# Performance work log

Hardware: AMD Instinct MI355X
Metric: run time of the kernel (lower is better)

## Reference

```python
import jax, jax.numpy as jnp
import numpy as np

B, I, T = 256, 64, 16
V, E, H = 4096, 256, 256


def setup_inputs() -> dict:
    key = jax.random.key(0)
    ks = jax.random.split(key, 12)
    emb = jax.random.normal(ks[0], (V, E), jnp.float32) * 0.02
    emb = emb.at[0].set(0.0)  # padding_idx=0
    s_e = 1.0 / np.sqrt(H)
    inp = {
        "batched_blocks": jax.random.randint(ks[1], (B, I, T), 0, V, jnp.int32),
        "actual_instr_counts": jax.random.randint(ks[2], (B,), 1, I + 1, jnp.int32),
        "actual_token_counts": jax.random.randint(ks[3], (B, I), 0, T + 1, jnp.int32),
        "embedding": emb,
        "Wih_tok": jax.random.uniform(ks[4], (4 * H, E), jnp.float32, -s_e, s_e),
        "Whh_tok": jax.random.uniform(ks[5], (4 * H, H), jnp.float32, -s_e, s_e),
        "b_tok": jax.random.uniform(ks[6], (4 * H,), jnp.float32, -s_e, s_e),
        "Wih_ins": jax.random.uniform(ks[7], (4 * H, H), jnp.float32, -s_e, s_e),
        "Whh_ins": jax.random.uniform(ks[8], (4 * H, H), jnp.float32, -s_e, s_e),
        "b_ins": jax.random.uniform(ks[9], (4 * H,), jnp.float32, -s_e, s_e),
        "linW": jax.random.uniform(ks[10], (1, H), jnp.float32, -s_e, s_e),
        "linb": jax.random.uniform(ks[11], (1,), jnp.float32, -s_e, s_e),
    }
    return inp


def _lstm_last(x, lengths, Wih, Whh, b):
    # x: [N, T, D]; returns hidden state at step lengths-1 (zeros if length==0),
    # matching pack_padded_sequence -> LSTM -> h_n semantics.
    N, Tt, _ = x.shape
    Hh = Whh.shape[1]

    def step(carry, xt):
        h, c = carry
        g = xt @ Wih.T + h @ Whh.T + b  # [N, 4H], torch gate order i,f,g,o
        i, f, gg, o = jnp.split(g, 4, axis=-1)
        c = jax.nn.sigmoid(f) * c + jax.nn.sigmoid(i) * jnp.tanh(gg)
        h = jax.nn.sigmoid(o) * jnp.tanh(c)
        return (h, c), h

    h0 = jnp.zeros((N, Hh), x.dtype)
    _, hs = jax.lax.scan(step, (h0, h0), jnp.swapaxes(x, 0, 1))  # [T, N, H]
    hs = jnp.swapaxes(hs, 0, 1)  # [N, T, H]
    idx = jnp.clip(lengths - 1, 0, Tt - 1).astype(jnp.int32)
    h_last = jnp.take_along_axis(hs, jnp.broadcast_to(idx[:, None, None], (N, 1, Hh)), axis=1)[:, 0]
    return jnp.where((lengths > 0)[:, None], h_last, jnp.zeros_like(h_last))


def reference(batched_blocks, actual_instr_counts, actual_token_counts,
              embedding, Wih_tok, Whh_tok, b_tok, Wih_ins, Whh_ins, b_ins,
              linW, linb):
    Bb, Ii, Tt = batched_blocks.shape
    tok_flat = batched_blocks.reshape(Bb * Ii, Tt)
    emb = embedding[tok_flat]  # [B*I, T, E]
    tok_len = actual_token_counts.reshape(-1)
    instr_repr = _lstm_last(emb, tok_len, Wih_tok, Whh_tok, b_tok)  # [B*I, H]
    instr_repr = instr_repr.reshape(Bb, Ii, -1)
    block_repr = _lstm_last(instr_repr, actual_instr_counts, Wih_ins, Whh_ins, b_ins)  # [B, H]
    return block_repr @ linW.T + linb  # [B, 1]
```

## Files before the change

kernel.cpp:

```cpp
#include <hip/hip_runtime.h>
#include <hip/hip_bf16.h>

#define Bq 256
#define Iq 64
#define Tq 16
#define Vq 4096
#define Eq 256
#define Hq 256
#define NSEQ 16384
#define HSTR 264
#define HR 272
#define HBUF 4352
#define CL 8
#define XCC_GETREG_IMM 6164

typedef __attribute__((ext_vector_type(8))) __bf16 bf16x8;
typedef __attribute__((ext_vector_type(8))) short short8;
typedef __attribute__((ext_vector_type(4))) float f32x4;

__device__ __forceinline__ bf16x8 as_bf8(short8 v) {
    union { short8 s; bf16x8 b; } u; u.s = v; return u.b;
}
__device__ __forceinline__ float sigf(float x) {
    return __builtin_amdgcn_rcpf(1.f + __expf(-x));
}
__device__ __forceinline__ float tanh_fast(float x) {
    float e = __expf(2.f * x);
    return 1.f - 2.f * __builtin_amdgcn_rcpf(e + 1.f);
}
__device__ __forceinline__ short bf16_rne(float x) {
    unsigned u = __float_as_uint(x);
    unsigned r = (u + 0x7fffu + ((u >> 16) & 1u)) >> 16;
    return (short)r;
}
__device__ __forceinline__ float bf16f(short h) {
    return __uint_as_float(((unsigned)(unsigned short)h) << 16);
}
__device__ __forceinline__ void gl_lds16(const unsigned* g, unsigned* l) {
    __builtin_amdgcn_global_load_lds(
        (const __attribute__((address_space(1))) void*)g,
        (__attribute__((address_space(3))) void*)l, 16, 0, 1);
}

__global__ void k_pack(const float* __restrict__ Wih_tok,
                       const float* __restrict__ b_tok,
                       const float* __restrict__ b_ins,
                       float* __restrict__ Wih4t,
                       float* __restrict__ b4t, float* __restrict__ b4i) {
    int g = blockIdx.x;
    int q = g >> 8;
    int j = g & 255;
    int k = threadIdx.x;
    Wih4t[(k * 256 + j) * 4 + q] = Wih_tok[g * Hq + k];
    if (k == 0) {
        b4t[j * 4 + q] = b_tok[g];
        b4i[j * 4 + q] = b_ins[g];
    }
}

__global__ void k_packB(const float* __restrict__ W0,
                        const float* __restrict__ W1,
                        short* __restrict__ B0h, short* __restrict__ B0l,
                        short* __restrict__ B1h, short* __restrict__ B1l) {
    int nt = blockIdx.x;
    int kc = blockIdx.y;
    int l  = threadIdx.x;
    int n = nt * 16 + (l & 15);
    int kb = kc * 32 + (l >> 4) * 8;
    size_t ob = ((size_t)(nt * 8 + kc) * 64 + l) * 8;
    #pragma unroll
    for (int m = 0; m < 8; ++m) {
        float v = W0[n * 256 + kb + m];
        short hi = bf16_rne(v);
        B0h[ob + m] = hi; B0l[ob + m] = bf16_rne(v - bf16f(hi));
        v = W1[n * 256 + kb + m];
        hi = bf16_rne(v);
        B1h[ob + m] = hi; B1l[ob + m] = bf16_rne(v - bf16f(hi));
    }
}

__global__ void k_packB2(const float* __restrict__ W2,
                         short* __restrict__ B2h, short* __restrict__ B2l) {
    int bx = blockIdx.x;
    int kc = blockIdx.y;
    int l  = threadIdx.x;
    int j  = bx >> 3, nt = bx & 7;
    int n_local = nt * 16 + (l & 15);
    int gate = n_local & 3;
    int u = j * 32 + (n_local >> 2);
    int row = gate * 256 + u;
    int kb = kc * 32 + (l >> 4) * 8;
    size_t ob = ((size_t)(bx * 8 + kc) * 64 + l) * 8;
    #pragma unroll
    for (int m = 0; m < 8; ++m) {
        float v = W2[row * 256 + kb + m];
        short hi = bf16_rne(v);
        B2h[ob + m] = hi;
        B2l[ob + m] = bf16_rne(v - bf16f(hi));
    }
}

__global__ __launch_bounds__(1024) void k_sortn(const int* __restrict__ len,
                                                int* __restrict__ perm,
                                                int n, int nbins) {
    __shared__ int cnt[65];
    __shared__ int base[65];
    int tid = threadIdx.x;
    if (tid < nbins) cnt[tid] = 0;
    __syncthreads();
    for (int i = tid; i < n; i += 1024) atomicAdd(&cnt[len[i]], 1);
    __syncthreads();
    if (tid == 0) {
        int acc = 0;
        for (int b = nbins - 1; b >= 0; --b) { base[b] = acc; acc += cnt[b]; }
    }
    __syncthreads();
    for (int i = tid; i < n; i += 1024) {
        int pos = atomicAdd(&base[len[i]], 1);
        perm[pos] = i;
    }
}

__global__ void k_zero(int* __restrict__ p, int n) {
    int i = blockIdx.x * blockDim.x + threadIdx.x;
    if (i < n) p[i] = 0;
}

__global__ __launch_bounds__(256) void k_epre(const float* __restrict__ emb,
                                              const float4* __restrict__ Wih4t,
                                              const float4* __restrict__ b4t,
                                              float4* __restrict__ Ep4) {
    __shared__ float es[8][Eq];
    int tid = threadIdx.x;
    int v0 = blockIdx.x * 8;
    #pragma unroll
    for (int r = 0; r < 8; ++r) es[r][tid] = emb[(v0 + r) * Eq + tid];
    __syncthreads();
    float4 a[8];
    #pragma unroll
    for (int r = 0; r < 8; ++r) a[r] = make_float4(0.f, 0.f, 0.f, 0.f);
    const float4* Wp = Wih4t + tid;
    #pragma unroll 2
    for (int k = 0; k < Eq; ++k) {
        float4 wv = Wp[k * 256];
        #pragma unroll
        for (int r = 0; r < 8; ++r) {
            float e = es[r][k];
            a[r].x += wv.x * e; a[r].y += wv.y * e;
            a[r].z += wv.z * e; a[r].w += wv.w * e;
        }
    }
    float4 b4 = b4t[tid];
    #pragma unroll
    for (int r = 0; r < 8; ++r) {
        Ep4[(size_t)(v0 + r) * 256 + tid] =
            make_float4(a[r].x + b4.x, a[r].y + b4.y, a[r].z + b4.z, a[r].w + b4.w);
    }
}

#define MFMA3(accv, ah, al, bh, bl) \
    accv = __builtin_amdgcn_mfma_f32_16x16x32_bf16(ah, bh, accv, 0, 0, 0); \
    accv = __builtin_amdgcn_mfma_f32_16x16x32_bf16(al, bh, accv, 0, 0, 0); \
    accv = __builtin_amdgcn_mfma_f32_16x16x32_bf16(ah, bl, accv, 0, 0, 0);

__global__ __launch_bounds__(512) void k_token_mfma(
        const int* __restrict__ tokens,
        const int* __restrict__ tok_len,
        const int* __restrict__ perm,
        const float4* __restrict__ Ep4,
        const short* __restrict__ Bhi, const short* __restrict__ Blo,
        const short* __restrict__ BXhi, const short* __restrict__ BXlo,
        const float4* __restrict__ b4i,
        float4* __restrict__ Xp4) {
    __shared__ __align__(16) short hb[2][32 * HSTR];
    __shared__ int toks[32][Tq];
    __shared__ int lens[32];
    __shared__ int sid[32];
    int tid  = threadIdx.x;
    int w    = tid >> 6;
    int lane = tid & 63;
    int l15  = lane & 15;
    int quad = lane >> 4;
    int s0   = blockIdx.x * 32;

    if (tid < 32) {
        int q = perm[s0 + tid];
        sid[tid]  = q;
        lens[tid] = tok_len[q];
    }
    {
        int* hz = (int*)&hb[0][0];
        for (int i = tid; i < 32 * HSTR; i += 512) hz[i] = 0;
    }
    __syncthreads();
    toks[tid >> 4][tid & 15] = tokens[sid[tid >> 4] * Tq + (tid & 15)];
    int lenr[2][4], sidr[2][4];
    #pragma unroll
    for (int mt = 0; mt < 2; ++mt)
        #pragma unroll
        for (int r = 0; r < 4; ++r) {
            lenr[mt][r] = lens[mt * 16 + quad * 4 + r];
            sidr[mt][r] = sid[mt * 16 + quad * 4 + r];
        }
    int tmax = 0;
    #pragma unroll
    for (int s = 0; s < 32; ++s) tmax = max(tmax, lens[s]);
    __syncthreads();

    f32x4 acc[2][4][2];
    float cst[2][2][4], hst[2][2][4];
    #pragma unroll
    for (int u2 = 0; u2 < 2; ++u2)
        #pragma unroll
        for (int mt = 0; mt < 2; ++mt)
            #pragma unroll
            for (int r = 0; r < 4; ++r) { cst[u2][mt][r] = 0.f; hst[u2][mt][r] = 0.f; }

    for (int t = 0; t < tmax; ++t) {
        #pragma unroll
        for (int u2 = 0; u2 < 2; ++u2) {
            int u = (w + u2 * 8) * 16 + l15;
            #pragma unroll
            for (int mt = 0; mt < 2; ++mt)
                #pragma unroll
                for (int r = 0; r < 4; ++r) {
                    float4 e = Ep4[(size_t)toks[mt * 16 + quad * 4 + r][t] * 256 + u];
                    acc[u2][0][mt][r] = e.x; acc[u2][1][mt][r] = e.y;
                    acc[u2][2][mt][r] = e.z; acc[u2][3][mt][r] = e.w;
                }
        }
        const short* hc0 = &hb[0][0];
        const short* hc1 = &hb[1][0];
        #pragma unroll 1
        for (int kc = 0; kc < 8; ++kc) {
            bf16x8 a0h = *(const bf16x8*)(hc0 + l15 * HSTR + kc * 32 + quad * 8);
            bf16x8 a0l = *(const bf16x8*)(hc1 + l15 * HSTR + kc * 32 + quad * 8);
            bf16x8 a1h = *(const bf16x8*)(hc0 + (16 + l15) * HSTR + kc * 32 + quad * 8);
            bf16x8 a1l = *(const bf16x8*)(hc1 + (16 + l15) * HSTR + kc * 32 + quad * 8);
            #pragma unroll
            for (int u2 = 0; u2 < 2; ++u2)
                #pragma unroll
                for (int g = 0; g < 4; ++g) {
                    size_t bo = ((size_t)((g * 16 + w + u2 * 8) * 8 + kc)) * 512 + lane * 8;
                    bf16x8 bh = *(const bf16x8*)(Bhi + bo);
                    bf16x8 bl = *(const bf16x8*)(Blo + bo);
                    MFMA3(acc[u2][g][0], a0h, a0l, bh, bl)
                    MFMA3(acc[u2][g][1], a1h, a1l, bh, bl)
                }
        }
        __syncthreads();
        #pragma unroll
        for (int u2 = 0; u2 < 2; ++u2) {
            int u = (w + u2 * 8) * 16 + l15;
            #pragma unroll
            for (int mt = 0; mt < 2; ++mt)
                #pragma unroll
                for (int r = 0; r < 4; ++r) {
                    int s = mt * 16 + quad * 4 + r;
                    if (t < lenr[mt][r]) {
                        float cn = sigf(acc[u2][1][mt][r]) * cst[u2][mt][r]
                                 + sigf(acc[u2][0][mt][r]) * tanh_fast(acc[u2][2][mt][r]);
                        cst[u2][mt][r] = cn;
                        hst[u2][mt][r] = sigf(acc[u2][3][mt][r]) * tanh_fast(cn);
                    }
                    float hv = hst[u2][mt][r];
                    short hi = bf16_rne(hv);
                    hb[0][s * HSTR + u] = hi;
                    hb[1][s * HSTR + u] = bf16_rne(hv - bf16f(hi));
                }
        }
        __syncthreads();
    }

    #pragma unroll
    for (int u2 = 0; u2 < 2; ++u2) {
        float4 bb = b4i[(w + u2 * 8) * 16 + l15];
        #pragma unroll
        for (int mt = 0; mt < 2; ++mt)
            #pragma unroll
            for (int r = 0; r < 4; ++r) {
                acc[u2][0][mt][r] = bb.x; acc[u2][1][mt][r] = bb.y;
                acc[u2][2][mt][r] = bb.z; acc[u2][3][mt][r] = bb.w;
            }
    }
    {
        const short* hc0 = &hb[0][0];
        const short* hc1 = &hb[1][0];
        #pragma unroll 1
        for (int kc = 0; kc < 8; ++kc) {
            bf16x8 a0h = *(const bf16x8*)(hc0 + l15 * HSTR + kc * 32 + quad * 8);
            bf16x8 a0l = *(const bf16x8*)(hc1 + l15 * HSTR + kc * 32 + quad * 8);
            bf16x8 a1h = *(const bf16x8*)(hc0 + (16 + l15) * HSTR + kc * 32 + quad * 8);
            bf16x8 a1l = *(const bf16x8*)(hc1 + (16 + l15) * HSTR + kc * 32 + quad * 8);
            #pragma unroll
            for (int u2 = 0; u2 < 2; ++u2)
                #pragma unroll
                for (int g = 0; g < 4; ++g) {
                    size_t bo = ((size_t)((g * 16 + w + u2 * 8) * 8 + kc)) * 512 + lane * 8;
                    bf16x8 bh = *(const bf16x8*)(BXhi + bo);
                    bf16x8 bl = *(const bf16x8*)(BXlo + bo);
                    MFMA3(acc[u2][g][0], a0h, a0l, bh, bl)
                    MFMA3(acc[u2][g][1], a1h, a1l, bh, bl)
                }
        }
    }
    #pragma unroll
    for (int u2 = 0; u2 < 2; ++u2) {
        int u = (w + u2 * 8) * 16 + l15;
        #pragma unroll
        for (int mt = 0; mt < 2; ++mt)
            #pragma unroll
            for (int r = 0; r < 4; ++r) {
                Xp4[(size_t)sidr[mt][r] * 256 + u] =
                    make_float4(acc[u2][0][mt][r], acc[u2][1][mt][r],
                                acc[u2][2][mt][r], acc[u2][3][mt][r]);
            }
    }
}

__global__ __launch_bounds__(256) void k_instr_xcd(
        const float* __restrict__ XpF,
        const int* __restrict__ instr_cnt,
        const int* __restrict__ perm2,
        const short* __restrict__ B2h, const short* __restrict__ B2l,
        int* __restrict__ xcd_cnt,
        int* __restrict__ flags,
        unsigned* __restrict__ hG,
        const float* __restrict__ linW,
        const float* __restrict__ linb,
        float* __restrict__ out) {
    __shared__ __align__(16) short Bs[2][32768];
    __shared__ __align__(16) unsigned hS[HBUF];
    __shared__ int lens[16], sid[16], role[2];
    int tid  = threadIdx.x;
    int w    = tid >> 6;
    int lane = tid & 63;
    int l15  = lane & 15;
    int quad = lane >> 4;

    if (tid == 0) {
        int xcd = __builtin_amdgcn_s_getreg(XCC_GETREG_IMM) & 7;
        int slot = atomicAdd(&xcd_cnt[xcd], 1);
        role[0] = xcd; role[1] = slot;
    }
    __syncthreads();
    int slot = role[1];
    if (slot >= 16) return;
    int c = role[0] * 2 + (slot >> 3);
    int j = slot & 7;

    if (tid < 16) {
        int q = perm2[c * 16 + tid];
        sid[tid]  = q;
        lens[tid] = instr_cnt[q];
    }
    {
        const float4* s0 = (const float4*)(B2h + (size_t)j * 32768);
        const float4* s1 = (const float4*)(B2l + (size_t)j * 32768);
        float4* d0 = (float4*)&Bs[0][0];
        float4* d1 = (float4*)&Bs[1][0];
        for (int i = tid; i < 4096; i += 256) { d0[i] = s0[i]; d1[i] = s1[i]; }
    }
    __syncthreads();
    int tmax = 0;
    #pragma unroll
    for (int s = 0; s < 16; ++s) tmax = max(tmax, lens[s]);
    int lenr[4], sidr[4];
    #pragma unroll
    for (int r = 0; r < 4; ++r) { lenr[r] = lens[quad * 4 + r]; sidr[r] = sid[quad * 4 + r]; }

    float cst[2][4], hst[2][4];
    #pragma unroll
    for (int r = 0; r < 4; ++r) { cst[0][r] = cst[1][r] = 0.f; hst[0][r] = hst[1][r] = 0.f; }
    int T0 = 2 * w, T1 = 2 * w + 1;
    unsigned* hGc = hG + (size_t)c * (4 * HBUF);
    int* flg = flags + c * 65 * 8;
    int gbase = l15 & ~3;

    for (int t = 0; t < tmax; ++t) {
        f32x4 acc0, acc1;
        #pragma unroll
        for (int r = 0; r < 4; ++r) {
            size_t base = ((size_t)sidr[r] * Iq + t) * 1024 + j * 128;
            acc0[r] = XpF[base + T0 * 16 + l15];
            acc1[r] = XpF[base + T1 * 16 + l15];
        }
        if (t > 0) {
            const volatile int* fp = flg + (t - 1) * 8;
            int cap = 0;
            while (true) {
                int ok = (lane < 8) ? (fp[lane] != 0) : 1;
                if (__all(ok)) break;
                if (++cap > (1 << 22)) break;
                __builtin_amdgcn_s_sleep(1);
            }
        }
        {
            const unsigned* hRdG = hGc + (size_t)(t & 3) * HBUF;
            #pragma unroll
            for (int rr = 0; rr < 4; ++rr)
                gl_lds16(hRdG + (rr * 256 + tid) * 4, hS + (rr * 256 + tid) * 4);
            if (tid < 64) gl_lds16(hRdG + (1024 + tid) * 4, hS + (1024 + tid) * 4);
        }
        __syncthreads();
        const unsigned* hrow = hS + l15 * HR;
        #pragma unroll
        for (int kc = 0; kc < 8; ++kc) {
            unsigned hp[8];
            *(uint4*)&hp[0] = *(const uint4*)(hrow + kc * 32 + quad * 8);
            *(uint4*)&hp[4] = *(const uint4*)(hrow + kc * 32 + quad * 8 + 4);
            short8 vhi, vlo;
            #pragma unroll
            for (int m = 0; m < 8; ++m) {
                vhi[m] = (short)(hp[m] & 0xffffu);
                vlo[m] = (short)(hp[m] >> 16);
            }
            bf16x8 ahi = as_bf8(vhi), alo = as_bf8(vlo);
            bf16x8 bh0 = *(const bf16x8*)(&Bs[0][((T0 * 8 + kc) * 64 + lane) * 8]);
            bf16x8 bl0 = *(const bf16x8*)(&Bs[1][((T0 * 8 + kc) * 64 + lane) * 8]);
            bf16x8 bh1 = *(const bf16x8*)(&Bs[0][((T1 * 8 + kc) * 64 + lane) * 8]);
            bf16x8 bl1 = *(const bf16x8*)(&Bs[1][((T1 * 8 + kc) * 64 + lane) * 8]);
            acc0 = __builtin_amdgcn_mfma_f32_16x16x32_bf16(ahi, bh0, acc0, 0, 0, 0);
            acc0 = __builtin_amdgcn_mfma_f32_16x16x32_bf16(alo, bh0, acc0, 0, 0, 0);
            acc0 = __builtin_amdgcn_mfma_f32_16x16x32_bf16(ahi, bl0, acc0, 0, 0, 0);
            acc1 = __builtin_amdgcn_mfma_f32_16x16x32_bf16(ahi, bh1, acc1, 0, 0, 0);
            acc1 = __builtin_amdgcn_mfma_f32_16x16x32_bf16(alo, bh1, acc1, 0, 0, 0);
            acc1 = __builtin_amdgcn_mfma_f32_16x16x32_bf16(ahi, bl1, acc1, 0, 0, 0);
        }
        unsigned* hWr = hGc + (size_t)((t + 1) & 3) * HBUF;
        #pragma unroll
        for (int r = 0; r < 4; ++r) {
            float v0 = acc0[r], v1 = acc1[r];
            float gi0 = __shfl(v0, gbase + 0, 16), gf0 = __shfl(v0, gbase + 1, 16);
            float gg0 = __shfl(v0, gbase + 2, 16), go0 = __shfl(v0, gbase + 3, 16);
            float gi1 = __shfl(v1, gbase + 0, 16), gf1 = __shfl(v1, gbase + 1, 16);
            float gg1 = __shfl(v1, gbase + 2, 16), go1 = __shfl(v1, gbase + 3, 16);
            if (t < lenr[r]) {
                float cn0 = sigf(gf0) * cst[0][r] + sigf(gi0) * tanh_fast(gg0);
                cst[0][r] = cn0;
                hst[0][r] = sigf(go0) * tanh_fast(cn0);
                float cn1 = sigf(gf1) * cst[1][r] + sigf(gi1) * tanh_fast(gg1);
                cst[1][r] = cn1;
                hst[1][r] = sigf(go1) * tanh_fast(cn1);
            }
        }
        if ((l15 & 3) == 0) {
            int u0 = 32 * j + 4 * T0 + (l15 >> 2);
            int u1 = 32 * j + 4 * T1 + (l15 >> 2);
            #pragma unroll
            for (int r = 0; r < 4; ++r) {
                int s = quad * 4 + r;
                float h0 = hst[0][r], h1 = hst[1][r];
                short h0h = bf16_rne(h0), h1h = bf16_rne(h1);
                unsigned p0 = (unsigned)(unsigned short)h0h |
                              ((unsigned)(unsigned short)bf16_rne(h0 - bf16f(h0h)) << 16);
                unsigned p1 = (unsigned)(unsigned short)h1h |
                              ((unsigned)(unsigned short)bf16_rne(h1 - bf16f(h1h)) << 16);
                hWr[s * HR + u0] = p0;
                hWr[s * HR + u1] = p1;
            }
        }
        __syncthreads();
        if (tid == 0) *(volatile int*)(flg + t * 8 + j) = 1;
    }

    if (j == 0) {
        const volatile int* fp = flg + (tmax - 1) * 8;
        int cap = 0;
        while (true) {
            int ok = (lane < 8) ? (fp[lane] != 0) : 1;
            if (__all(ok)) break;
            if (++cap > (1 << 22)) break;
            __builtin_amdgcn_s_sleep(1);
        }
        const unsigned* hRdG = hGc + (size_t)(tmax & 3) * HBUF;
        #pragma unroll
        for (int rr = 0; rr < 4; ++rr)
            gl_lds16(hRdG + (rr * 256 + tid) * 4, hS + (rr * 256 + tid) * 4);
        if (tid < 64) gl_lds16(hRdG + (1024 + tid) * 4, hS + (1024 + tid) * 4);
        __syncthreads();
        int s = tid >> 4, k0 = (tid & 15) * 16;
        float p = 0.f;
        #pragma unroll
        for (int m = 0; m < 16; ++m) {
            int u = k0 + m;
            unsigned pk = hS[s * HR + u];
            float hv = bf16f((short)(pk & 0xffffu)) + bf16f((short)(pk >> 16));
            p += linW[u] * hv;
        }
        p += __shfl_down(p, 8, 16);
        p += __shfl_down(p, 4, 16);
        p += __shfl_down(p, 2, 16);
        p += __shfl_down(p, 1, 16);
        if ((tid & 15) == 0) out[sid[s]] = p + linb[0];
    }
}

extern "C" void kernel_launch(void* const* d_in, const int* in_sizes, int n_in,
                              void* d_out, int out_size, void* d_ws, size_t ws_size,
                              hipStream_t stream) {
    const int*   tokens  = (const int*)d_in[0];
    const int*   icnt    = (const int*)d_in[1];
    const int*   tcnt    = (const int*)d_in[2];
    const float* emb     = (const float*)d_in[3];
    const float* Wih_tok = (const float*)d_in[4];
    const float* Whh_tok = (const float*)d_in[5];
    const float* b_tok   = (const float*)d_in[6];
    const float* Wih_ins = (const float*)d_in[7];
    const float* Whh_ins = (const float*)d_in[8];
    const float* b_ins   = (const float*)d_in[9];
    const float* linW    = (const float*)d_in[10];
    const float* linb    = (const float*)d_in[11];
    float* out = (float*)d_out;

    float* ws_f    = (float*)d_ws;
    float* Wih4t   = ws_f;
    float* b4t     = Wih4t + 262144;
    float* b4i     = b4t + 1024;
    int*   perm    = (int*)(b4i + 1024);
    int*   perm2   = perm + 16384;
    int*   xcd_cnt = perm2 + 256;
    int*   flags   = xcd_cnt + 8;
    int*   sync_end= flags + 8320;
    short* Bhi     = (short*)(sync_end + 376);
    short* Blo     = Bhi + 262144;
    short* BXhi    = Blo + 262144;
    short* BXlo    = BXhi + 262144;
    short* B2h     = BXlo + 262144;
    short* B2l     = B2h + 262144;
    unsigned* hG   = (unsigned*)(B2l + 262144);
    float* Ep4     = (float*)(hG + 278528);
    float* Xp4     = Ep4 + 4194304;

    size_t need = ((char*)(Xp4 + 16777216)) - ((char*)d_ws);
    if (ws_size < need) return;

    hipLaunchKernelGGL(k_pack, dim3(1024), dim3(256), 0, stream,
                       Wih_tok, b_tok, b_ins, Wih4t, b4t, b4i);
    hipLaunchKernelGGL(k_packB, dim3(64, 8), dim3(64), 0, stream,
                       Whh_tok, Wih_ins, Bhi, Blo, BXhi, BXlo);
    hipLaunchKernelGGL(k_packB2, dim3(64, 8), dim3(64), 0, stream,
                       Whh_ins, B2h, B2l);
    hipLaunchKernelGGL(k_sortn, dim3(1), dim3(1024), 0, stream, tcnt, perm, NSEQ, 17);
    hipLaunchKernelGGL(k_sortn, dim3(1), dim3(1024), 0, stream, icnt, perm2, Bq, 65);
    hipLaunchKernelGGL(k_zero, dim3(33), dim3(256), 0, stream, xcd_cnt, 8328);
    hipLaunchKernelGGL(k_zero, dim3(1088), dim3(256), 0, stream, (int*)hG, 278528);
    hipLaunchKernelGGL(k_epre, dim3(512), dim3(256), 0, stream,
                       emb, (const float4*)Wih4t, (const float4*)b4t, (float4*)Ep4);
    hipLaunchKernelGGL(k_token_mfma, dim3(512), dim3(512), 0, stream,
                       tokens, tcnt, perm, (const float4*)Ep4,
                       Bhi, Blo, BXhi, BXlo, (const float4*)b4i, (float4*)Xp4);
    hipLaunchKernelGGL(k_instr_xcd, dim3(256), dim3(256), 0, stream,
                       Xp4, icnt, perm2, B2h, B2l, xcd_cnt, flags, hG,
                       linW, linb, out);
}
```

Baseline: 801.6 us.

## Retile token LSTM kernel to 64 sequences per block with 1024 threads

The token-LSTM MFMA kernel now handles 64 sorted sequences per block using 16 waves, each owning one 16-column hidden slice across four 16-row M tiles. Before, 8 waves each handled two slices for 32 sequences. Each weight fragment loaded from global memory is now reused across four M tiles instead of two, halving per-sequence weight traffic. Lengths are packed into bytes and tmax is read as lens[0], which relies on the perm being sorted descending. The cost is fewer blocks (256), more LDS per block and higher register pressure under the 1024-thread bound, which may cause spills or lower occupancy.

```diff
diff --git a/kernel.cpp b/kernel.cpp
--- a/kernel.cpp
+++ b/kernel.cpp
@@ -163,7 +163,7 @@
     accv = __builtin_amdgcn_mfma_f32_16x16x32_bf16(al, bh, accv, 0, 0, 0); \
     accv = __builtin_amdgcn_mfma_f32_16x16x32_bf16(ah, bl, accv, 0, 0, 0);
 
-__global__ __launch_bounds__(512) void k_token_mfma(
+__global__ __launch_bounds__(1024) void k_token_mfma(
         const int* __restrict__ tokens,
         const int* __restrict__ tok_len,
         const int* __restrict__ perm,
@@ -172,115 +172,106 @@
         const short* __restrict__ BXhi, const short* __restrict__ BXlo,
         const float4* __restrict__ b4i,
         float4* __restrict__ Xp4) {
-    __shared__ __align__(16) short hb[2][32 * HSTR];
-    __shared__ int toks[32][Tq];
-    __shared__ int lens[32];
-    __shared__ int sid[32];
+    __shared__ __align__(16) short hb[2][64 * HSTR];
+    __shared__ int toks[64][Tq];
+    __shared__ int lens[64];
+    __shared__ int sid[64];
     int tid  = threadIdx.x;
     int w    = tid >> 6;
     int lane = tid & 63;
     int l15  = lane & 15;
     int quad = lane >> 4;
-    int s0   = blockIdx.x * 32;
-
-    if (tid < 32) {
+    int s0   = blockIdx.x * 64;
+    int u    = w * 16 + l15;
+
+    if (tid < 64) {
         int q = perm[s0 + tid];
         sid[tid]  = q;
         lens[tid] = tok_len[q];
     }
     {
         int* hz = (int*)&hb[0][0];
-        for (int i = tid; i < 32 * HSTR; i += 512) hz[i] = 0;
+        for (int i = tid; i < 64 * HSTR; i += 1024) hz[i] = 0;
     }
     __syncthreads();
     toks[tid >> 4][tid & 15] = tokens[sid[tid >> 4] * Tq + (tid & 15)];
-    int lenr[2][4], sidr[2][4];
-    #pragma unroll
-    for (int mt = 0; mt < 2; ++mt)
-        #pragma unroll
-        for (int r = 0; r < 4; ++r) {
-            lenr[mt][r] = lens[mt * 16 + quad * 4 + r];
-            sidr[mt][r] = sid[mt * 16 + quad * 4 + r];
-        }
-    int tmax = 0;
-    #pragma unroll
-    for (int s = 0; s < 32; ++s) tmax = max(tmax, lens[s]);
-    __syncthreads();
-
-    f32x4 acc[2][4][2];
-    float cst[2][2][4], hst[2][2][4];
-    #pragma unroll
-    for (int u2 = 0; u2 < 2; ++u2)
-        #pragma unroll
-        for (int mt = 0; mt < 2; ++mt)
-            #pragma unroll
-            for (int r = 0; r < 4; ++r) { cst[u2][mt][r] = 0.f; hst[u2][mt][r] = 0.f; }
+    unsigned lenp[4];
+    #pragma unroll
+    for (int mt = 0; mt < 4; ++mt) {
+        lenp[mt] = (unsigned)lens[mt * 16 + quad * 4 + 0]
+                 | ((unsigned)lens[mt * 16 + quad * 4 + 1] << 8)
+                 | ((unsigned)lens[mt * 16 + quad * 4 + 2] << 16)
+                 | ((unsigned)lens[mt * 16 + quad * 4 + 3] << 24);
+    }
+    int tmax = lens[0];
+    __syncthreads();
+
+    f32x4 acc[4][4];
+    float cst[4][4], hst[4][4];
+    #pragma unroll
+    for (int mt = 0; mt < 4; ++mt)
+        #pragma unroll
+        for (int r = 0; r < 4; ++r) { cst[mt][r] = 0.f; hst[mt][r] = 0.f; }
 
     for (int t = 0; t < tmax; ++t) {
         #pragma unroll
-        for (int u2 = 0; u2 < 2; ++u2) {
-            int u = (w + u2 * 8) * 16 + l15;
-            #pragma unroll
-            for (int mt = 0; mt < 2; ++mt)
-                #pragma unroll
-                for (int r = 0; r < 4; ++r) {
-                    float4 e = Ep4[(size_t)toks[mt * 16 + quad * 4 + r][t] * 256 + u];
-                    acc[u2][0][mt][r] = e.x; acc[u2][1][mt][r] = e.y;
-                    acc[u2][2][mt][r] = e.z; acc[u2][3][mt][r] = e.w;
-                }
-        }
+        for (int mt = 0; mt < 4; ++mt)
+            #pragma unroll
+            for (int r = 0; r < 4; ++r) {
+                float4 e = Ep4[(size_t)toks[mt * 16 + quad * 4 + r][t] * 256 + u];
+                acc[0][mt][r] = e.x; acc[1][mt][r] = e.y;
+                acc[2][mt][r] = e.z; acc[3][mt][r] = e.w;
+            }
         const short* hc0 = &hb[0][0];
         const short* hc1 = &hb[1][0];
         #pragma unroll 1
         for (int kc = 0; kc < 8; ++kc) {
-            bf16x8 a0h = *(const bf16x8*)(hc0 + l15 * HSTR + kc * 32 + quad * 8);
-            bf16x8 a0l = *(const bf16x8*)(hc1 + l15 * HSTR + kc * 32 + quad * 8);
-            bf16x8 a1h = *(const bf16x8*)(hc0 + (16 + l15) * HSTR + kc * 32 + quad * 8);
-            bf16x8 a1l = *(const bf16x8*)(hc1 + (16 + l15) * HSTR + kc * 32 + quad * 8);
-            #pragma unroll
-            for (int u2 = 0; u2 < 2; ++u2)
+            bf16x8 ah[4], al[4];
+            #pragma unroll
+            for (int mt = 0; mt < 4; ++mt) {
+                ah[mt] = *(const bf16x8*)(hc0 + (mt * 16 + l15) * HSTR + kc * 32 + quad * 8);
+                al[mt] = *(const bf16x8*)(hc1 + (mt * 16 + l15) * HSTR + kc * 32 + quad * 8);
+            }
+            #pragma unroll
+            for (int g = 0; g < 4; ++g) {
+                size_t bo = ((size_t)((g * 16 + w) * 8 + kc)) * 512 + lane * 8;
+                bf16x8 bh = *(const bf16x8*)(Bhi + bo);
+                bf16x8 bl = *(const bf16x8*)(Blo + bo);
                 #pragma unroll
-                for (int g = 0; g < 4; ++g) {
-                    size_t bo = ((size_t)((g * 16 + w + u2 * 8) * 8 + kc)) * 512 + lane * 8;
-                    bf16x8 bh = *(const bf16x8*)(Bhi + bo);
-                    bf16x8 bl = *(const bf16x8*)(Blo + bo);
-                    MFMA3(acc[u2][g][0], a0h, a0l, bh, bl)
-                    MFMA3(acc[u2][g][1], a1h, a1l, bh, bl)
+                for (int mt = 0; mt < 4; ++mt) {
+                    MFMA3(acc[g][mt], ah[mt], al[mt], bh, bl)
                 }
+            }
         }
         __syncthreads();
         #pragma unroll
-        for (int u2 = 0; u2 < 2; ++u2) {
-            int u = (w + u2 * 8) * 16 + l15;
-            #pragma unroll
-            for (int mt = 0; mt < 2; ++mt)
-                #pragma unroll
-                for (int r = 0; r < 4; ++r) {
-                    int s = mt * 16 + quad * 4 + r;
-                    if (t < lenr[mt][r]) {
-                        float cn = sigf(acc[u2][1][mt][r]) * cst[u2][mt][r]
-                                 + sigf(acc[u2][0][mt][r]) * tanh_fast(acc[u2][2][mt][r]);
-                        cst[u2][mt][r] = cn;
-                        hst[u2][mt][r] = sigf(acc[u2][3][mt][r]) * tanh_fast(cn);
-                    }
-                    float hv = hst[u2][mt][r];
-                    short hi = bf16_rne(hv);
-                    hb[0][s * HSTR + u] = hi;
-                    hb[1][s * HSTR + u] = bf16_rne(hv - bf16f(hi));
+        for (int mt = 0; mt < 4; ++mt)
+            #pragma unroll
+            for (int r = 0; r < 4; ++r) {
+                int s = mt * 16 + quad * 4 + r;
+                int lr = (int)((lenp[mt] >> (8 * r)) & 255u);
+                if (t < lr) {
+                    float cn = sigf(acc[1][mt][r]) * cst[mt][r]
+                             + sigf(acc[0][mt][r]) * tanh_fast(acc[2][mt][r]);
+                    cst[mt][r] = cn;
+                    hst[mt][r] = sigf(acc[3][mt][r]) * tanh_fast(cn);
                 }
-        }
+                float hv = hst[mt][r];
+                short hi = bf16_rne(hv);
+                hb[0][s * HSTR + u] = hi;
+                hb[1][s * HSTR + u] = bf16_rne(hv - bf16f(hi));
+            }
         __syncthreads();
     }
 
-    #pragma unroll
-    for (int u2 = 0; u2 < 2; ++u2) {
-        float4 bb = b4i[(w + u2 * 8) * 16 + l15];
-        #pragma unroll
-        for (int mt = 0; mt < 2; ++mt)
+    {
+        float4 bb = b4i[u];
+        #pragma unroll
+        for (int mt = 0; mt < 4; ++mt)
             #pragma unroll
             for (int r = 0; r < 4; ++r) {
-                acc[u2][0][mt][r] = bb.x; acc[u2][1][mt][r] = bb.y;
-                acc[u2][2][mt][r] = bb.z; acc[u2][3][mt][r] = bb.w;
+                acc[0][mt][r] = bb.x; acc[1][mt][r] = bb.y;
+                acc[2][mt][r] = bb.z; acc[3][mt][r] = bb.w;
             }
     }
     {
@@ -288,34 +279,33 @@
         const short* hc1 = &hb[1][0];
         #pragma unroll 1
         for (int kc = 0; kc < 8; ++kc) {
-            bf16x8 a0h = *(const bf16x8*)(hc0 + l15 * HSTR + kc * 32 + quad * 8);
-            bf16x8 a0l = *(const bf16x8*)(hc1 + l15 * HSTR + kc * 32 + quad * 8);
-            bf16x8 a1h = *(const bf16x8*)(hc0 + (16 + l15) * HSTR + kc * 32 + quad * 8);
-            bf16x8 a1l = *(const bf16x8*)(hc1 + (16 + l15) * HSTR + kc * 32 + quad * 8);
-            #pragma unroll
-            for (int u2 = 0; u2 < 2; ++u2)
+            bf16x8 ah[4], al[4];
+            #pragma unroll
+            for (int mt = 0; mt < 4; ++mt) {
+                ah[mt] = *(const bf16x8*)(hc0 + (mt * 16 + l15) * HSTR + kc * 32 + quad * 8);
+                al[mt] = *(const bf16x8*)(hc1 + (mt * 16 + l15) * HSTR + kc * 32 + quad * 8);
+            }
+            #pragma unroll
+            for (int g = 0; g < 4; ++g) {
+                size_t bo = ((size_t)((g * 16 + w) * 8 + kc)) * 512 + lane * 8;
+                bf16x8 bh = *(const bf16x8*)(BXhi + bo);
+                bf16x8 bl = *(const bf16x8*)(BXlo + bo);
                 #pragma unroll
-                for (int g = 0; g < 4; ++g) {
-                    size_t bo = ((size_t)((g * 16 + w + u2 * 8) * 8 + kc)) * 512 + lane * 8;
-                    bf16x8 bh = *(const bf16x8*)(BXhi + bo);
-                    bf16x8 bl = *(const bf16x8*)(BXlo + bo);
-                    MFMA3(acc[u2][g][0], a0h, a0l, bh, bl)
-                    MFMA3(acc[u2][g][1], a1h, a1l, bh, bl)
+                for (int mt = 0; mt < 4; ++mt) {
+                    MFMA3(acc[g][mt], ah[mt], al[mt], bh, bl)
                 }
-        }
-    }
-    #pragma unroll
-    for (int u2 = 0; u2 < 2; ++u2) {
-        int u = (w + u2 * 8) * 16 + l15;
-        #pragma unroll
-        for (int mt = 0; mt < 2; ++mt)
-            #pragma unroll
-            for (int r = 0; r < 4; ++r) {
-                Xp4[(size_t)sidr[mt][r] * 256 + u] =
-                    make_float4(acc[u2][0][mt][r], acc[u2][1][mt][r],
-                                acc[u2][2][mt][r], acc[u2][3][mt][r]);
-            }
-    }
+            }
+        }
+    }
+    #pragma unroll
+    for (int mt = 0; mt < 4; ++mt)
+        #pragma unroll
+        for (int r = 0; r < 4; ++r) {
+            int s = mt * 16 + quad * 4 + r;
+            Xp4[(size_t)sid[s] * 256 + u] =
+                make_float4(acc[0][mt][r], acc[1][mt][r],
+                            acc[2][mt][r], acc[3][mt][r]);
+        }
 }
 
 __global__ __launch_bounds__(256) void k_instr_xcd(
@@ -547,7 +537,7 @@
     hipLaunchKernelGGL(k_zero, dim3(1088), dim3(256), 0, stream, (int*)hG, 278528);
     hipLaunchKernelGGL(k_epre, dim3(512), dim3(256), 0, stream,
                        emb, (const float4*)Wih4t, (const float4*)b4t, (float4*)Ep4);
-    hipLaunchKernelGGL(k_token_mfma, dim3(512), dim3(512), 0, stream,
+    hipLaunchKernelGGL(k_token_mfma, dim3(256), dim3(1024), 0, stream,
                        tokens, tcnt, perm, (const float4*)Ep4,
                        Bhi, Blo, BXhi, BXlo, (const float4*)b4i, (float4*)Xp4);
     hipLaunchKernelGGL(k_instr_xcd, dim3(256), dim3(256), 0, stream,
```

Result: slower. 1.035 ms (+29.1%).
